# Performance work log

Hardware: AMD Instinct MI355X
Metric: run time of the kernel (lower is better)

Reference implementation:

```python
import jax, jax.numpy as jnp
import numpy as np

B, L, S, DIM, H, DH, DFF = 2, 2048, 2048, 1024, 16, 64, 4096
EPS = 1e-6


def _ln(x, w, b):
    m = jnp.mean(x, axis=-1, keepdims=True)
    v = jnp.mean(jnp.square(x - m), axis=-1, keepdims=True)
    return (x - m) / jnp.sqrt(v + EPS) * w + b


def _mha(q, k, v, mask):
    # q: [B,L,H*DH], k/v: [B,S,H*DH], mask broadcastable to [B,H,L,S], True = masked
    b, l, _ = q.shape
    s = k.shape[1]
    q = q.reshape(b, l, H, DH)
    k = k.reshape(b, s, H, DH)
    v = v.reshape(b, s, H, DH)
    scale = 1.0 / np.sqrt(DH).astype(np.float32)
    attn = jnp.einsum('blhd,bshd->bhls', q, k) * scale
    if mask is not None:
        attn = jnp.where(mask, -jnp.inf, attn)
    attn = jax.nn.softmax(attn, axis=-1)
    out = jnp.einsum('bhls,bshd->blhd', attn, v)
    return out.reshape(b, l, H * DH)


def setup_inputs() -> dict:
    key = jax.random.key(0)
    ks = jax.random.split(key, 12)
    std = 0.02
    inp = {
        'input': jax.random.normal(ks[0], (B, L, DIM), jnp.float32),
        'source': jax.random.normal(ks[1], (B, S, DIM), jnp.float32),
        # source mask: no source positions masked
        'source_mask': jnp.zeros((B, 1, 1, S), bool),
        # causal mask for self-attention (True above diagonal -> masked)
        'mask': jnp.triu(jnp.ones((L, L), bool), 1)[None, None],
        # self-attention
        'ln_self_w': jnp.ones((DIM,), jnp.float32),
        'ln_self_b': jnp.zeros((DIM,), jnp.float32),
        'w_qkv': std * jax.random.normal(ks[2], (DIM, 3 * DIM), jnp.float32),
        'b_qkv': jnp.zeros((3 * DIM,), jnp.float32),
        'w_so': std * jax.random.normal(ks[3], (DIM, DIM), jnp.float32),
        'b_so': jnp.zeros((DIM,), jnp.float32),
        # cross-attention
        'ln_cross_w': jnp.ones((DIM,), jnp.float32),
        'ln_cross_b': jnp.zeros((DIM,), jnp.float32),
        'w_q': std * jax.random.normal(ks[4], (DIM, DIM), jnp.float32),
        'b_q': jnp.zeros((DIM,), jnp.float32),
        'w_kv': std * jax.random.normal(ks[5], (DIM, 2 * DIM), jnp.float32),
        'b_kv': jnp.zeros((2 * DIM,), jnp.float32),
        'w_co': std * jax.random.normal(ks[6], (DIM, DIM), jnp.float32),
        'b_co': jnp.zeros((DIM,), jnp.float32),
        # MLP (1 layer)
        'ln_mlp_w': jnp.ones((DIM,), jnp.float32),
        'ln_mlp_b': jnp.zeros((DIM,), jnp.float32),
        'w_ff1': std * jax.random.normal(ks[7], (DIM, DFF), jnp.float32),
        'b_ff1': jnp.zeros((DFF,), jnp.float32),
        'w_ff2': std * jax.random.normal(ks[8], (DFF, DIM), jnp.float32),
        'b_ff2': jnp.zeros((DIM,), jnp.float32),
    }
    return inp


def reference(input, source, source_mask, mask,
              ln_self_w, ln_self_b, w_qkv, b_qkv, w_so, b_so,
              ln_cross_w, ln_cross_b, w_q, b_q, w_kv, b_kv, w_co, b_co,
              ln_mlp_w, ln_mlp_b, w_ff1, b_ff1, w_ff2, b_ff2):
    x = input
    # self-attention block (pre-LN)
    h = _ln(x, ln_self_w, ln_self_b)
    qkv = h @ w_qkv + b_qkv
    q, k, v = jnp.split(qkv, 3, axis=-1)
    sa = _mha(q, k, v, mask) @ w_so + b_so
    x = x + sa
    # cross-attention block (pre-LN)
    h = _ln(x, ln_cross_w, ln_cross_b)
    q = h @ w_q + b_q
    kv = source @ w_kv + b_kv
    k, v = jnp.split(kv, 2, axis=-1)
    ca = _mha(q, k, v, source_mask) @ w_co + b_co
    x = x + ca
    # feed-forward block (pre-LN), eval mode (no dropout/droppath)
    h = _ln(x, ln_mlp_w, ln_mlp_b)
    ff = jax.nn.gelu(h @ w_ff1 + b_ff1, approximate=False) @ w_ff2 + b_ff2
    x = x + ff
    return x
```

## Files before the change

kernel.cpp:

```cpp
#include <hip/hip_runtime.h>
#include <hip/hip_bf16.h>
#include <math.h>

typedef __bf16 bf16_t;
typedef __bf16 bf16x8 __attribute__((ext_vector_type(8)));
typedef __bf16 bf16x4 __attribute__((ext_vector_type(4)));
typedef float  f32x4  __attribute__((ext_vector_type(4)));

#define DIM   1024
#define NB    2
#define NL    2048
#define NS    2048
#define NH    16
#define NDH   64
#define NDFF  4096

#define DS_READ_B128(dst, addr) \
    asm volatile("ds_read_b128 %0, %1" : "=v"(dst) : "v"(addr))
#define LGKM0_FENCE() do { \
    asm volatile("s_waitcnt lgkmcnt(0)" ::: "memory"); \
    __builtin_amdgcn_sched_barrier(0); } while (0)

__device__ __forceinline__ bf16x8 ld_bf16x8(const bf16_t* p) {
    return *reinterpret_cast<const bf16x8*>(p);
}

__device__ __forceinline__ void gl_lds16(const bf16_t* g, bf16_t* l) {
    __builtin_amdgcn_global_load_lds(
        (const __attribute__((address_space(1))) void*)g,
        (__attribute__((address_space(3))) void*)l, 16, 0, 0);
}

__device__ __forceinline__ unsigned lds_u32(const bf16_t* p) {
    return (unsigned)(uintptr_t)(__attribute__((address_space(3))) const void*)p;
}

__global__ __launch_bounds__(256)
void wconv_kernel(const float* __restrict__ in, bf16_t* __restrict__ out, int K, int N)
{
    __shared__ float tile[32][33];
    int n0 = blockIdx.x * 32, k0 = blockIdx.y * 32;
    int tx = threadIdx.x & 31, ty = threadIdx.x >> 5;
    #pragma unroll
    for (int j = 0; j < 4; ++j)
        tile[ty + 8*j][tx] = in[(size_t)(k0 + ty + 8*j) * N + n0 + tx];
    __syncthreads();
    #pragma unroll
    for (int j = 0; j < 4; ++j)
        out[(size_t)(n0 + ty + 8*j) * K + k0 + tx] = (bf16_t)tile[tx][ty + 8*j];
}

__global__ __launch_bounds__(256)
void f2b_kernel(const float* __restrict__ in, bf16_t* __restrict__ out)
{
    size_t i = ((size_t)blockIdx.x * 256 + threadIdx.x) * 4;
    float4 v = *reinterpret_cast<const float4*>(in + i);
    bf16x4 o = { (bf16_t)v.x, (bf16_t)v.y, (bf16_t)v.z, (bf16_t)v.w };
    *reinterpret_cast<bf16x4*>(out + i) = o;
}

__global__ __launch_bounds__(256)
void ln_kernel(const float* __restrict__ x, const float* __restrict__ wgt,
               const float* __restrict__ bia, bf16_t* __restrict__ out)
{
    int row = blockIdx.x, tid = threadIdx.x;
    float4 xv = reinterpret_cast<const float4*>(x + (size_t)row * DIM)[tid];
    float s1 = xv.x + xv.y + xv.z + xv.w;
    float s2 = xv.x*xv.x + xv.y*xv.y + xv.z*xv.z + xv.w*xv.w;
    #pragma unroll
    for (int off = 32; off > 0; off >>= 1) {
        s1 += __shfl_xor(s1, off, 64);
        s2 += __shfl_xor(s2, off, 64);
    }
    __shared__ float red[8];
    int w = tid >> 6;
    if ((tid & 63) == 0) { red[w] = s1; red[w + 4] = s2; }
    __syncthreads();
    s1 = red[0] + red[1] + red[2] + red[3];
    s2 = red[4] + red[5] + red[6] + red[7];
    float mean = s1 * (1.0f / DIM);
    float var  = s2 * (1.0f / DIM) - mean * mean;
    float rstd = rsqrtf(var + 1e-6f);
    float4 wv = reinterpret_cast<const float4*>(wgt)[tid];
    float4 bv = reinterpret_cast<const float4*>(bia)[tid];
    bf16x4 o = { (bf16_t)((xv.x - mean) * rstd * wv.x + bv.x),
                 (bf16_t)((xv.y - mean) * rstd * wv.y + bv.y),
                 (bf16_t)((xv.z - mean) * rstd * wv.z + bv.z),
                 (bf16_t)((xv.w - mean) * rstd * wv.w + bv.w) };
    reinterpret_cast<bf16x4*>(out + (size_t)row * DIM)[tid] = o;
}

template<int EPI, int BM, int BN>
__global__ __launch_bounds__(256)
void gemm_kernel(const bf16_t* __restrict__ A, const bf16_t* __restrict__ BT,
                 const float* __restrict__ bias, const float* __restrict__ res,
                 void* __restrict__ out, int M, int N, int K)
{
    constexpr int WM = BM / 2, WN = BN / 2;
    constexpr int AM = WM / 16, AN = WN / 16;
    constexpr int ABE = (BM + BN) * 32;
    constexpr int LPS = (BM + BN) / 64;
    __shared__ __align__(16) bf16_t lds[3 * ABE];

    int tid = threadIdx.x;
    int lane = tid & 63, w = tid >> 6;
    int wr = w >> 1, wc = w & 1;
    int la = lane & 15, lg = lane >> 4;

    int gx = gridDim.x;
    int flat = blockIdx.y * gx + blockIdx.x;
    int cpx = gx >> 3;
    int xcd = flat & 7, loc = flat >> 3;
    int m0 = (loc / cpx) * BM;
    int n0 = (xcd * cpx + loc % cpx) * BN;

    f32x4 acc[AM][AN] = {};

    int sr = lane >> 2;
    int sc = ((lane & 3) ^ ((lane >> 3) & 3)) * 8;
    const bf16_t* Ap = A  + (size_t)(m0 + w * (BM / 4) + sr) * K + sc;
    const bf16_t* Bp = BT + (size_t)(n0 + w * (BN / 4) + sr) * K + sc;

    auto stage = [&](int t, int buf) {
        int k0 = t * 32;
        bf16_t* base = &lds[buf * ABE];
        #pragma unroll
        for (int i = 0; i < BM / 64; ++i)
            gl_lds16(Ap + ((size_t)i * 16) * K + k0, base + (w * (BM / 4) + i * 16) * 32);
        #pragma unroll
        for (int i = 0; i < BN / 64; ++i)
            gl_lds16(Bp + ((size_t)i * 16) * K + k0, base + (BM + w * (BN / 4) + i * 16) * 32);
    };

    unsigned ldsb = lds_u32(lds);
    unsigned kla = (la >> 1) & 3;
    unsigned a_base = ldsb + ((wr * WM + la) * 32 + (lg ^ kla) * 8) * 2;
    unsigned b_base = ldsb + (BM * 32 + (wc * WN + la) * 32 + (lg ^ kla) * 8) * 2;

    auto compute = [&](int buf) {
        unsigned dB = (unsigned)(buf * ABE * 2);
        bf16x8 af[AM], bfr[AN];
        #pragma unroll
        for (int mi = 0; mi < AM; ++mi)
            DS_READ_B128(af[mi], a_base + dB + mi * 1024);
        #pragma unroll
        for (int ni = 0; ni < AN; ++ni)
            DS_READ_B128(bfr[ni], b_base + dB + ni * 1024);
        LGKM0_FENCE();
        __builtin_amdgcn_s_setprio(1);
        #pragma unroll
        for (int mi = 0; mi < AM; ++mi)
            #pragma unroll
            for (int ni = 0; ni < AN; ++ni)
                acc[mi][ni] = __builtin_amdgcn_mfma_f32_16x16x32_bf16(
                                  af[mi], bfr[ni], acc[mi][ni], 0, 0, 0);
        __builtin_amdgcn_s_setprio(0);
    };

    int nt = K / 32;
    stage(0, 0);
    stage(1, 1);
    int buf = 0;
    for (int t = 0; t < nt - 1; ++t) {
        asm volatile("s_waitcnt vmcnt(%0)" :: "n"(LPS) : "memory");
        __builtin_amdgcn_s_barrier();
        __builtin_amdgcn_sched_barrier(0);
        if (t + 2 < nt) stage(t + 2, (t + 2) % 3);
        compute(buf);
        buf = (buf == 2) ? 0 : buf + 1;
    }
    asm volatile("s_waitcnt vmcnt(0)" ::: "memory");
    __builtin_amdgcn_s_barrier();
    __builtin_amdgcn_sched_barrier(0);
    compute(buf);

    #pragma unroll
    for (int mi = 0; mi < AM; ++mi) {
        #pragma unroll
        for (int ni = 0; ni < AN; ++ni) {
            #pragma unroll
            for (int i = 0; i < 4; ++i) {
                int row = m0 + wr * WM + mi * 16 + lg * 4 + i;
                int col = n0 + wc * WN + ni * 16 + la;
                float v = acc[mi][ni][i] + bias[col];
                if (EPI == 1) v = 0.5f * v * (1.0f + erff(v * 0.70710678118f));
                if (EPI == 2)
                    ((float*)out)[(size_t)row * N + col] = res[(size_t)row * N + col] + v;
                else
                    ((bf16_t*)out)[(size_t)row * N + col] = (bf16_t)v;
            }
        }
    }
}

template<bool CAUSAL>
__global__ __launch_bounds__(256)
void attn_kernel(const bf16_t* __restrict__ Q, int qs,
                 const bf16_t* __restrict__ Kp, int ks,
                 const bf16_t* __restrict__ Vp, int vs,
                 bf16_t* __restrict__ O, int os, int L, int S)
{
    __shared__ __align__(16) bf16_t Ks[64 * 64];
    __shared__ __align__(16) bf16_t Vt[64 * 64];
    __shared__ __align__(16) bf16_t Ps[4][32 * 64];

    int tid = threadIdx.x, lane = tid & 63, w = tid >> 6;
    int la = lane & 15, lg = lane >> 4;
    int qtile = (CAUSAL ? (gridDim.x - 1 - blockIdx.x) : blockIdx.x) * 128;
    int b = blockIdx.y >> 4, h = blockIdx.y & 15;

    const bf16_t* qb = Q  + (size_t)(b * L) * qs + h * 64;
    const bf16_t* kb = Kp + (size_t)(b * S) * ks + h * 64;
    const bf16_t* vb = Vp + (size_t)(b * S) * vs + h * 64;
    bf16_t*       ob = O  + (size_t)(b * L) * os + h * 64;

    bf16x8 qf[2][2];
    #pragma unroll
    for (int rg = 0; rg < 2; ++rg) {
        int qrow = qtile + w * 32 + rg * 16 + la;
        qf[rg][0] = ld_bf16x8(qb + (size_t)qrow * qs + lg * 8);
        qf[rg][1] = ld_bf16x8(qb + (size_t)qrow * qs + 32 + lg * 8);
        #pragma unroll
        for (int j = 0; j < 8; ++j) {
            qf[rg][0][j] = qf[rg][0][j] * (bf16_t)0.125f;
            qf[rg][1][j] = qf[rg][1][j] * (bf16_t)0.125f;
        }
    }

    f32x4 zero = {0.f, 0.f, 0.f, 0.f};
    f32x4 o[2][4];
    #pragma unroll
    for (int rg = 0; rg < 2; ++rg)
        #pragma unroll
        for (int dt = 0; dt < 4; ++dt) o[rg][dt] = zero;
    float lpart[2][4] = {};

    int rk  = tid >> 3;
    int ck8 = tid & 7;
    int sv0   = tid & 31;
    int dbase = (tid >> 5) * 8;
    int r7 = la & 7;

    int n_full = (CAUSAL ? qtile : S) / 64;
    int nit = n_full + (CAUSAL ? 2 : 0);

    bf16x8 kr0 = ld_bf16x8(kb + (size_t)rk * ks + ck8 * 8);
    bf16x8 kr1 = ld_bf16x8(kb + (size_t)(rk + 32) * ks + ck8 * 8);
    bf16x8 vr0 = ld_bf16x8(vb + (size_t)sv0 * vs + dbase);
    bf16x8 vr1 = ld_bf16x8(vb + (size_t)(sv0 + 32) * vs + dbase);

    for (int it = 0; it < nit; ++it) {
        int s0 = it * 64;
        bool diag = CAUSAL && (it >= n_full);

        __syncthreads();
        *reinterpret_cast<bf16x8*>(&Ks[rk * 64 + ((ck8 ^ (rk & 7)) * 8)]) = kr0;
        *reinterpret_cast<bf16x8*>(&Ks[(rk + 32) * 64 + ((ck8 ^ (rk & 7)) * 8)]) = kr1;
        #pragma unroll
        for (int j = 0; j < 8; ++j) {
            Vt[(dbase + j) * 64 + (sv0 ^ (j << 3))]        = vr0[j];
            Vt[(dbase + j) * 64 + ((sv0 + 32) ^ (j << 3))] = vr1[j];
        }
        __syncthreads();

        if (it + 1 < nit) {
            int s1 = s0 + 64;
            kr0 = ld_bf16x8(kb + (size_t)(s1 + rk) * ks + ck8 * 8);
            kr1 = ld_bf16x8(kb + (size_t)(s1 + rk + 32) * ks + ck8 * 8);
            vr0 = ld_bf16x8(vb + (size_t)(s1 + sv0) * vs + dbase);
            vr1 = ld_bf16x8(vb + (size_t)(s1 + sv0 + 32) * vs + dbase);
        }

        f32x4 sf[2][4];
        #pragma unroll
        for (int ct = 0; ct < 4; ++ct) {
            const bf16_t* kr = &Ks[(ct * 16 + la) * 64];
            bf16x8 k0 = ld_bf16x8(kr + ((lg ^ r7) * 8));
            bf16x8 k1 = ld_bf16x8(kr + (((4 + lg) ^ r7) * 8));
            #pragma unroll
            for (int rg = 0; rg < 2; ++rg) {
                f32x4 z = zero;
                z = __builtin_amdgcn_mfma_f32_16x16x32_bf16(qf[rg][0], k0, z, 0, 0, 0);
                z = __builtin_amdgcn_mfma_f32_16x16x32_bf16(qf[rg][1], k1, z, 0, 0, 0);
                sf[rg][ct] = z;
            }
        }

        #pragma unroll
        for (int rg = 0; rg < 2; ++rg) {
            #pragma unroll
            for (int ct = 0; ct < 4; ++ct) {
                #pragma unroll
                for (int i = 0; i < 4; ++i) {
                    float p = __expf(sf[rg][ct][i]);
                    if (diag) {
                        int sg = s0 + ct * 16 + la;
                        int qg = qtile + w * 32 + rg * 16 + lg * 4 + i;
                        if (sg > qg) p = 0.f;
                    }
                    lpart[rg][i] += p;
                    int row = rg * 16 + lg * 4 + i;
                    Ps[w][row * 64 + ((ct * 16 + la) ^ ((row & 7) << 3))] = (bf16_t)p;
                }
            }
        }

        bf16x8 pa[2][2];
        #pragma unroll
        for (int rg = 0; rg < 2; ++rg) {
            const bf16_t* pr = &Ps[w][(rg * 16 + la) * 64];
            pa[rg][0] = ld_bf16x8(pr + ((lg ^ r7) * 8));
            pa[rg][1] = ld_bf16x8(pr + (((4 + lg) ^ r7) * 8));
        }
        #pragma unroll
        for (int dt = 0; dt < 4; ++dt) {
            const bf16_t* vr = &Vt[(dt * 16 + la) * 64];
            bf16x8 v0 = ld_bf16x8(vr + ((lg ^ r7) * 8));
            bf16x8 v1 = ld_bf16x8(vr + (((4 + lg) ^ r7) * 8));
            #pragma unroll
            for (int rg = 0; rg < 2; ++rg) {
                o[rg][dt] = __builtin_amdgcn_mfma_f32_16x16x32_bf16(pa[rg][0], v0, o[rg][dt], 0, 0, 0);
                o[rg][dt] = __builtin_amdgcn_mfma_f32_16x16x32_bf16(pa[rg][1], v1, o[rg][dt], 0, 0, 0);
            }
        }
    }

    #pragma unroll
    for (int off = 1; off < 16; off <<= 1)
        #pragma unroll
        for (int rg = 0; rg < 2; ++rg)
            #pragma unroll
            for (int i = 0; i < 4; ++i)
                lpart[rg][i] += __shfl_xor(lpart[rg][i], off, 64);

    #pragma unroll
    for (int rg = 0; rg < 2; ++rg)
        #pragma unroll
        for (int dt = 0; dt < 4; ++dt)
            #pragma unroll
            for (int i = 0; i < 4; ++i) {
                int row = qtile + w * 32 + rg * 16 + lg * 4 + i;
                float val = o[rg][dt][i] / lpart[rg][i];
                ob[(size_t)row * os + dt * 16 + la] = (bf16_t)val;
            }
}

extern "C" void kernel_launch(void* const* d_in, const int* in_sizes, int n_in,
                              void* d_out, int out_size, void* d_ws, size_t ws_size,
                              hipStream_t stream)
{
    const float* input     = (const float*)d_in[0];
    const float* source    = (const float*)d_in[1];
    const float* ln_self_w = (const float*)d_in[4];
    const float* ln_self_b = (const float*)d_in[5];
    const float* w_qkv     = (const float*)d_in[6];
    const float* b_qkv     = (const float*)d_in[7];
    const float* w_so      = (const float*)d_in[8];
    const float* b_so      = (const float*)d_in[9];
    const float* ln_cross_w= (const float*)d_in[10];
    const float* ln_cross_b= (const float*)d_in[11];
    const float* w_q       = (const float*)d_in[12];
    const float* b_q       = (const float*)d_in[13];
    const float* w_kv      = (const float*)d_in[14];
    const float* b_kv      = (const float*)d_in[15];
    const float* w_co      = (const float*)d_in[16];
    const float* b_co      = (const float*)d_in[17];
    const float* ln_mlp_w  = (const float*)d_in[18];
    const float* ln_mlp_b  = (const float*)d_in[19];
    const float* w_ff1     = (const float*)d_in[20];
    const float* b_ff1     = (const float*)d_in[21];
    const float* w_ff2     = (const float*)d_in[22];
    const float* b_ff2     = (const float*)d_in[23];

    const int M = NB * NL;

    char* ws = (char*)d_ws;
    size_t off = 0;
    auto alloc = [&](size_t bytes) { char* p = ws + off; off += (bytes + 255) & ~(size_t)255; return p; };

    bf16_t* wT_qkv = (bf16_t*)alloc((size_t)3072 * 1024 * 2);
    bf16_t* wT_so  = (bf16_t*)alloc((size_t)1024 * 1024 * 2);
    bf16_t* wT_q   = (bf16_t*)alloc((size_t)1024 * 1024 * 2);
    bf16_t* wT_kv  = (bf16_t*)alloc((size_t)2048 * 1024 * 2);
    bf16_t* wT_co  = (bf16_t*)alloc((size_t)1024 * 1024 * 2);
    bf16_t* wT_ff1 = (bf16_t*)alloc((size_t)4096 * 1024 * 2);
    bf16_t* wT_ff2 = (bf16_t*)alloc((size_t)1024 * 4096 * 2);
    bf16_t* srcb   = (bf16_t*)alloc((size_t)M * 1024 * 2);
    bf16_t* hbuf   = (bf16_t*)alloc((size_t)M * 1024 * 2);
    bf16_t* qkvb   = (bf16_t*)alloc((size_t)M * 3072 * 2);
    bf16_t* attnb  = (bf16_t*)alloc((size_t)M * 1024 * 2);
    bf16_t* qcb    = (bf16_t*)alloc((size_t)M * 1024 * 2);
    bf16_t* kvcb   = (bf16_t*)alloc((size_t)M * 2048 * 2);
    float*  xbuf   = (float*) alloc((size_t)M * 1024 * 4);
    bf16_t* ff1b   = (bf16_t*)alloc((size_t)M * 4096 * 2);
    (void)ws_size; (void)n_in; (void)in_sizes; (void)out_size;

    wconv_kernel<<<dim3(3072/32, 1024/32), 256, 0, stream>>>(w_qkv, wT_qkv, 1024, 3072);
    wconv_kernel<<<dim3(1024/32, 1024/32), 256, 0, stream>>>(w_so,  wT_so,  1024, 1024);
    wconv_kernel<<<dim3(1024/32, 1024/32), 256, 0, stream>>>(w_q,   wT_q,   1024, 1024);
    wconv_kernel<<<dim3(2048/32, 1024/32), 256, 0, stream>>>(w_kv,  wT_kv,  1024, 2048);
    wconv_kernel<<<dim3(1024/32, 1024/32), 256, 0, stream>>>(w_co,  wT_co,  1024, 1024);
    wconv_kernel<<<dim3(4096/32, 1024/32), 256, 0, stream>>>(w_ff1, wT_ff1, 1024, 4096);
    wconv_kernel<<<dim3(1024/32, 4096/32), 256, 0, stream>>>(w_ff2, wT_ff2, 4096, 1024);
    f2b_kernel<<<(M * 1024) / (256 * 4), 256, 0, stream>>>(source, srcb);

    ln_kernel<<<M, 256, 0, stream>>>(input, ln_self_w, ln_self_b, hbuf);
    gemm_kernel<0,128,128><<<dim3(3072/128, M/128), 256, 0, stream>>>(hbuf, wT_qkv, b_qkv, nullptr, qkvb, M, 3072, 1024);
    attn_kernel<true><<<dim3(NL/128, NB*NH), 256, 0, stream>>>(qkvb, 3072, qkvb + 1024, 3072, qkvb + 2048, 3072,
                                                               attnb, 1024, NL, NL);
    gemm_kernel<2,128,64><<<dim3(1024/64, M/128), 256, 0, stream>>>(attnb, wT_so, b_so, input, xbuf, M, 1024, 1024);

    ln_kernel<<<M, 256, 0, stream>>>(xbuf, ln_cross_w, ln_cross_b, hbuf);
    gemm_kernel<0,128,64><<<dim3(1024/64, M/128), 256, 0, stream>>>(hbuf, wT_q, b_q, nullptr, qcb, M, 1024, 1024);
    gemm_kernel<0,128,128><<<dim3(2048/128, M/128), 256, 0, stream>>>(srcb, wT_kv, b_kv, nullptr, kvcb, M, 2048, 1024);
    attn_kernel<false><<<dim3(NL/128, NB*NH), 256, 0, stream>>>(qcb, 1024, kvcb, 2048, kvcb + 1024, 2048,
                                                                attnb, 1024, NL, NS);
    gemm_kernel<2,128,64><<<dim3(1024/64, M/128), 256, 0, stream>>>(attnb, wT_co, b_co, xbuf, xbuf, M, 1024, 1024);

    ln_kernel<<<M, 256, 0, stream>>>(xbuf, ln_mlp_w, ln_mlp_b, hbuf);
    gemm_kernel<1,128,128><<<dim3(4096/128, M/128), 256, 0, stream>>>(hbuf, wT_ff1, b_ff1, nullptr, ff1b, M, 4096, 1024);
    gemm_kernel<2,128,64><<<dim3(1024/64, M/128), 256, 0, stream>>>(ff1b, wT_ff2, b_ff2, xbuf, d_out, M, 1024, 4096);
}
```

Measured before the change: 417.2 us.

## Switch GEMM to BK=64 double-buffered LDS pipeline with 8-way XOR swizzle

```diff
diff --git a/kernel.cpp b/kernel.cpp
--- a/kernel.cpp
+++ b/kernel.cpp
@@ -98,9 +98,8 @@
 {
     constexpr int WM = BM / 2, WN = BN / 2;
     constexpr int AM = WM / 16, AN = WN / 16;
-    constexpr int ABE = (BM + BN) * 32;
-    constexpr int LPS = (BM + BN) / 64;
-    __shared__ __align__(16) bf16_t lds[3 * ABE];
+    constexpr int ABE = (BM + BN) * 64;
+    __shared__ __align__(16) bf16_t lds[2 * ABE];
 
     int tid = threadIdx.x;
     int lane = tid & 63, w = tid >> 6;
@@ -116,36 +115,52 @@
 
     f32x4 acc[AM][AN] = {};
 
-    int sr = lane >> 2;
-    int sc = ((lane & 3) ^ ((lane >> 3) & 3)) * 8;
-    const bf16_t* Ap = A  + (size_t)(m0 + w * (BM / 4) + sr) * K + sc;
-    const bf16_t* Bp = BT + (size_t)(n0 + w * (BN / 4) + sr) * K + sc;
+    int sr  = lane >> 3;
+    int sch = lane & 7;
+    int scol = ((sch ^ sr) * 8);
+    const bf16_t* Ap = A  + (size_t)(m0 + w * (BM / 4) + sr) * K + scol;
+    const bf16_t* Bp = BT + (size_t)(n0 + w * (BN / 4) + sr) * K + scol;
 
     auto stage = [&](int t, int buf) {
-        int k0 = t * 32;
+        int k0 = t * 64;
         bf16_t* base = &lds[buf * ABE];
         #pragma unroll
-        for (int i = 0; i < BM / 64; ++i)
-            gl_lds16(Ap + ((size_t)i * 16) * K + k0, base + (w * (BM / 4) + i * 16) * 32);
-        #pragma unroll
-        for (int i = 0; i < BN / 64; ++i)
-            gl_lds16(Bp + ((size_t)i * 16) * K + k0, base + (BM + w * (BN / 4) + i * 16) * 32);
+        for (int i = 0; i < BM / 32; ++i)
+            gl_lds16(Ap + ((size_t)i * 8) * K + k0, base + (w * (BM / 4) + i * 8) * 64);
+        #pragma unroll
+        for (int i = 0; i < BN / 32; ++i)
+            gl_lds16(Bp + ((size_t)i * 8) * K + k0, base + (BM + w * (BN / 4) + i * 8) * 64);
     };
 
     unsigned ldsb = lds_u32(lds);
-    unsigned kla = (la >> 1) & 3;
-    unsigned a_base = ldsb + ((wr * WM + la) * 32 + (lg ^ kla) * 8) * 2;
-    unsigned b_base = ldsb + (BM * 32 + (wc * WN + la) * 32 + (lg ^ kla) * 8) * 2;
+    unsigned kla = la & 7;
+    unsigned a_base = ldsb + (wr * WM + la) * 128 + ((lg ^ kla) * 16);
+    unsigned b_base = ldsb + BM * 128 + (wc * WN + la) * 128 + ((lg ^ kla) * 16);
 
     auto compute = [&](int buf) {
         unsigned dB = (unsigned)(buf * ABE * 2);
         bf16x8 af[AM], bfr[AN];
         #pragma unroll
         for (int mi = 0; mi < AM; ++mi)
-            DS_READ_B128(af[mi], a_base + dB + mi * 1024);
+            DS_READ_B128(af[mi], a_base + dB + mi * 2048);
         #pragma unroll
         for (int ni = 0; ni < AN; ++ni)
-            DS_READ_B128(bfr[ni], b_base + dB + ni * 1024);
+            DS_READ_B128(bfr[ni], b_base + dB + ni * 2048);
+        LGKM0_FENCE();
+        __builtin_amdgcn_s_setprio(1);
+        #pragma unroll
+        for (int mi = 0; mi < AM; ++mi)
+            #pragma unroll
+            for (int ni = 0; ni < AN; ++ni)
+                acc[mi][ni] = __builtin_amdgcn_mfma_f32_16x16x32_bf16(
+                                  af[mi], bfr[ni], acc[mi][ni], 0, 0, 0);
+        __builtin_amdgcn_s_setprio(0);
+        #pragma unroll
+        for (int mi = 0; mi < AM; ++mi)
+            DS_READ_B128(af[mi], (a_base + dB + mi * 2048) ^ 64u);
+        #pragma unroll
+        for (int ni = 0; ni < AN; ++ni)
+            DS_READ_B128(bfr[ni], (b_base + dB + ni * 2048) ^ 64u);
         LGKM0_FENCE();
         __builtin_amdgcn_s_setprio(1);
         #pragma unroll
@@ -157,22 +172,15 @@
         __builtin_amdgcn_s_setprio(0);
     };
 
-    int nt = K / 32;
+    int nt = K / 64;
     stage(0, 0);
-    stage(1, 1);
-    int buf = 0;
-    for (int t = 0; t < nt - 1; ++t) {
-        asm volatile("s_waitcnt vmcnt(%0)" :: "n"(LPS) : "memory");
+    for (int t = 0; t < nt; ++t) {
+        asm volatile("s_waitcnt vmcnt(0)" ::: "memory");
         __builtin_amdgcn_s_barrier();
         __builtin_amdgcn_sched_barrier(0);
-        if (t + 2 < nt) stage(t + 2, (t + 2) % 3);
-        compute(buf);
-        buf = (buf == 2) ? 0 : buf + 1;
+        if (t + 1 < nt) stage(t + 1, (t + 1) & 1);
+        compute(t & 1);
     }
-    asm volatile("s_waitcnt vmcnt(0)" ::: "memory");
-    __builtin_amdgcn_s_barrier();
-    __builtin_amdgcn_sched_barrier(0);
-    compute(buf);
 
     #pragma unroll
     for (int mi = 0; mi < AM; ++mi) {
```

Result: faster. 406.1 us (-2.7%).
